# Kernel optimization log

Measured on AMD Instinct MI355X. Metric: run time of the kernel, lower is better.

The kernel has to match this reference:

```python
import jax, jax.numpy as jnp
import numpy as np
import math

B, R, C = 4, 512, 512
E, H, D, M, F = 256, 16, 16, 16, 512  # embed, heads, qkv_dim, ms_hidden, ff_hidden
EPS = 1e-5


def setup_inputs() -> dict:
    key = jax.random.key(0)
    ks = jax.random.split(key, 20)
    s = lambda fan_in: 1.0 / math.sqrt(fan_in)
    u = lambda k, shape, lim: jax.random.uniform(k, shape, jnp.float32, -lim, lim)
    mix1_init = (1 / 2) ** 0.5
    mix2_init = (1 / 16) ** 0.5
    return {
        "row_emb": jax.random.normal(ks[0], (B, R, E), jnp.float32),
        "col_emb": jax.random.normal(ks[1], (B, C, E), jnp.float32),
        "cost_mat": jax.random.uniform(ks[2], (B, R, C), jnp.float32),
        "Wq": u(ks[3], (E, H * D), s(E)),
        "Wk": u(ks[4], (E, H * D), s(E)),
        "Wv": u(ks[5], (E, H * D), s(E)),
        "mix1_w": u(ks[6], (H, 2, M), mix1_init),
        "mix1_b": u(ks[7], (H, M), mix1_init),
        "mix2_w": u(ks[8], (H, M, 1), mix2_init),
        "mix2_b": u(ks[9], (H, 1), mix2_init),
        "Wc": u(ks[10], (H * D, E), s(H * D)),
        "bc": u(ks[11], (E,), s(H * D)),
        "W1": u(ks[12], (E, F), s(E)),
        "b1": u(ks[13], (F,), s(E)),
        "W2": u(ks[14], (F, E), s(F)),
        "b2": u(ks[15], (E,), s(F)),
        "g1": jnp.ones((E,), jnp.float32),
        "be1": jnp.zeros((E,), jnp.float32),
        "g2": jnp.ones((E,), jnp.float32),
        "be2": jnp.zeros((E,), jnp.float32),
    }


def _instance_norm(x, gamma, beta):
    # InstanceNorm1d on x permuted to (B, E, L): normalize over seq dim per (b, channel)
    mean = jnp.mean(x, axis=1, keepdims=True)          # [B,1,E]
    var = jnp.mean((x - mean) ** 2, axis=1, keepdims=True)
    return (x - mean) * jax.lax.rsqrt(var + EPS) * gamma + beta


def reference(row_emb, col_emb, cost_mat, Wq, Wk, Wv, mix1_w, mix1_b, mix2_w,
              mix2_b, Wc, bc, W1, b1, W2, b2, g1, be1, g2, be2):
    # QKV projections, split heads: [B,L,H*D] -> [B,H,L,D]
    q = (row_emb @ Wq).reshape(B, R, H, D).transpose(0, 2, 1, 3)
    k = (col_emb @ Wk).reshape(B, C, H, D).transpose(0, 2, 1, 3)
    v = (col_emb @ Wv).reshape(B, C, H, D).transpose(0, 2, 1, 3)

    dot = jnp.einsum('bhrd,bhcd->bhrc', q, k) / math.sqrt(D)
    cost = jnp.broadcast_to(cost_mat[:, None, :, :], (B, H, R, C))
    two = jnp.stack((dot, cost), axis=-1)               # [B,H,R,C,2]

    # per-head 2 -> M -> 1 mixing MLP over scores
    ms1 = jnp.einsum('bhrcs,hsm->bhrcm', two, mix1_w) + mix1_b[None, :, None, None, :]
    ms1 = jax.nn.relu(ms1)
    mixed = jnp.einsum('bhrcm,hm->bhrc', ms1, mix2_w[:, :, 0]) + mix2_b[:, 0][None, :, None, None]

    weights = jax.nn.softmax(mixed, axis=-1)            # [B,H,R,C]
    out = jnp.einsum('bhrc,bhcd->bhrd', weights, v)
    out_concat = out.transpose(0, 2, 1, 3).reshape(B, R, H * D)

    mh = out_concat @ Wc + bc                           # multi_head_combine

    # TransformerFFN with instance norm
    x = _instance_norm(row_emb + mh, g1, be1)
    ffn = jax.nn.relu(x @ W1 + b1) @ W2 + b2
    return _instance_norm(x + ffn, g2, be2)
```

## Files before the change

kernel.cpp:

```cpp
#include <hip/hip_runtime.h>
#include <hip/hip_bf16.h>

typedef __hip_bfloat16 bf16;
typedef __hip_bfloat162 bf162;
typedef _Float16 f16;
typedef __attribute__((ext_vector_type(2))) _Float16 h2;
typedef __attribute__((ext_vector_type(8))) short short8;
typedef __attribute__((ext_vector_type(4))) float f32x4;

#define B_ 4
#define R_ 512
#define C_ 512
#define E_ 256
#define H_ 16
#define D_ 16

__device__ __forceinline__ float b2f(bf16 x) { return __bfloat162float(x); }
__device__ __forceinline__ void stout(bf16* p, float v) { *p = __float2bfloat16(v); }
__device__ __forceinline__ void stout(f16* p, float v) { *p = (f16)v; }

template <int AMODE, typename OT, int BM, int BN, bool BIAS, int RES, bool RELU, bool STATS>
__device__ __forceinline__ void mfma_gemm_body(
    const void* __restrict__ Ap, const float* __restrict__ W, float bscl,
    const float* __restrict__ bias, const void* __restrict__ Res,
    const float* __restrict__ normS, const float* __restrict__ normG, const float* __restrict__ normB,
    float* __restrict__ statsOut, OT* __restrict__ Cout,
    int M, int N, int K, int bx, int by)
{
    constexpr int MT = BM / 32, NT = BN / 32;
    constexpr int AEL = BM * 64 / 256, BEL = BN * 64 / 256;
    __shared__ __align__(16) bf16 As[BM * 80];
    __shared__ __align__(16) bf16 Bs[BN * 80];
    const int tid = threadIdx.x;
    const int wid = tid >> 6, lane = tid & 63;
    const int wm = wid >> 1, wn = wid & 1;
    const int fr = lane & 15, quad = lane >> 4;
    const int m0 = by * BM, n0 = bx * BN;
    const int arow = (AEL == 16) ? (tid >> 2) : (tid >> 3);
    const int akg  = (AEL == 16) ? ((tid & 3) << 4) : ((tid & 7) << 3);
    const int brow = (BEL == 16) ? (tid >> 2) : (tid >> 3);
    const int bkg  = (BEL == 16) ? ((tid & 3) << 4) : ((tid & 7) << 3);

    f32x4 acc[MT][NT];
#pragma unroll
    for (int mt = 0; mt < MT; mt++)
#pragma unroll
        for (int nt = 0; nt < NT; nt++) acc[mt][nt] = (f32x4){0.f, 0.f, 0.f, 0.f};

    for (int k0 = 0; k0 < K; k0 += 64) {
        if constexpr (AMODE == 0) {
            const short8* gp = (const short8*)((const bf16*)Ap + (size_t)(m0 + arow) * K + k0 + akg);
#pragma unroll
            for (int t8 = 0; t8 < AEL / 8; t8++) *(short8*)(&As[arow * 80 + akg + 8 * t8]) = gp[t8];
        } else if constexpr (AMODE == 1) {
            const float4* gp = (const float4*)((const float*)Ap + (size_t)(m0 + arow) * K + k0 + akg);
#pragma unroll
            for (int j = 0; j < AEL / 4; j++) {
                const float4 f = gp[j];
                *(bf162*)(&As[arow * 80 + akg + j * 4])     = __float22bfloat162_rn(make_float2(f.x, f.y));
                *(bf162*)(&As[arow * 80 + akg + j * 4 + 2]) = __float22bfloat162_rn(make_float2(f.z, f.w));
            }
        } else {
            const int bb = (m0 + arow) >> 9;
            const bf16* ap = (const bf16*)Ap + (size_t)(m0 + arow) * K + k0 + akg;
            bf16 tmp[AEL];
#pragma unroll
            for (int t8 = 0; t8 < AEL / 8; t8++) *(short8*)(tmp + 8 * t8) = ((const short8*)ap)[t8];
#pragma unroll
            for (int j = 0; j < AEL; j++) {
                const int e = k0 + akg + j;
                const float s = normS[bb * 256 + e], sq = normS[1024 + bb * 256 + e];
                const float mn = s * (1.f / 512.f);
                float var = sq * (1.f / 512.f) - mn * mn; var = fmaxf(var, 0.f);
                As[arow * 80 + akg + j] = __float2bfloat16(
                    (b2f(tmp[j]) - mn) * rsqrtf(var + 1e-5f) * normG[e] + normB[e]);
            }
        }
        {
#pragma unroll
            for (int j = 0; j < BEL; j++)
                Bs[brow * 80 + bkg + j] = __float2bfloat16(
                    bscl * W[(size_t)(k0 + bkg + j) * N + (n0 + brow)]);
        }
        __syncthreads();

        short8 af[MT][2], bfr[NT][2];
#pragma unroll
        for (int mt = 0; mt < MT; mt++) {
            const int ar = wm * (BM / 2) + mt * 16 + fr;
#pragma unroll
            for (int kh = 0; kh < 2; kh++)
                af[mt][kh] = *(const short8*)(&As[ar * 80 + quad * 8 + kh * 32]);
        }
#pragma unroll
        for (int nt = 0; nt < NT; nt++) {
            const int br = wn * (BN / 2) + nt * 16 + fr;
#pragma unroll
            for (int kh = 0; kh < 2; kh++)
                bfr[nt][kh] = *(const short8*)(&Bs[br * 80 + quad * 8 + kh * 32]);
        }
#pragma unroll
        for (int kh = 0; kh < 2; kh++)
#pragma unroll
            for (int mt = 0; mt < MT; mt++)
#pragma unroll
                for (int nt = 0; nt < NT; nt++)
                    acc[mt][nt] = __builtin_amdgcn_mfma_f32_16x16x32_bf16(
                        af[mt][kh], bfr[nt][kh], acc[mt][nt], 0, 0, 0);
        __syncthreads();
    }

    float vsum[NT], vss[NT];
#pragma unroll
    for (int nt = 0; nt < NT; nt++) { vsum[nt] = 0.f; vss[nt] = 0.f; }
#pragma unroll
    for (int mt = 0; mt < MT; mt++) {
#pragma unroll
        for (int nt = 0; nt < NT; nt++) {
#pragma unroll
            for (int i = 0; i < 4; i++) {
                const int row = m0 + wm * (BM / 2) + mt * 16 + quad * 4 + i;
                const int col = n0 + wn * (BN / 2) + nt * 16 + fr;
                float v = acc[mt][nt][i];
                if (BIAS) v += bias[col];
                if constexpr (RES == 1) v += ((const float*)Res)[(size_t)row * N + col];
                if constexpr (RES == 3) {
                    const int bb = row >> 9;
                    const float yv = b2f(((const bf16*)Res)[(size_t)row * N + col]);
                    const float s = normS[bb * 256 + col], sq = normS[1024 + bb * 256 + col];
                    const float mn = s * (1.f / 512.f);
                    float var = sq * (1.f / 512.f) - mn * mn; var = fmaxf(var, 0.f);
                    v += (yv - mn) * rsqrtf(var + 1e-5f) * normG[col] + normB[col];
                }
                if (RELU) v = fmaxf(v, 0.f);
                stout(&Cout[(size_t)row * N + col], v);
                if (STATS) { vsum[nt] += v; vss[nt] += v * v; }
            }
        }
    }
    if constexpr (STATS) {
        float* sred = (float*)As;
#pragma unroll
        for (int nt = 0; nt < NT; nt++) {
            float a = vsum[nt]; a += __shfl_xor(a, 16, 64); a += __shfl_xor(a, 32, 64);
            float c = vss[nt];  c += __shfl_xor(c, 16, 64); c += __shfl_xor(c, 32, 64);
            if (quad == 0) {
                const int cl = wn * (BN / 2) + nt * 16 + fr;
                sred[wm * (2 * BN) + cl * 2 + 0] = a;
                sred[wm * (2 * BN) + cl * 2 + 1] = c;
            }
        }
        __syncthreads();
        if (tid < 2 * BN) {
            const int cl = tid >> 1, w = tid & 1;
            const float tot = sred[cl * 2 + w] + sred[2 * BN + cl * 2 + w];
            atomicAdd(&statsOut[w * 1024 + (m0 >> 9) * 256 + n0 + cl], tot);
        }
    }
}

template <int AMODE, typename OT, int BM, int BN, bool BIAS, int RES, bool RELU, bool STATS>
__global__ __launch_bounds__(256) void mfma_gemm_kernel(
    const void* __restrict__ Ap, const float* __restrict__ W, float bscl,
    const float* __restrict__ bias, const void* __restrict__ Res,
    const float* __restrict__ normS, const float* __restrict__ normG, const float* __restrict__ normB,
    float* __restrict__ statsOut, OT* __restrict__ Cout, int M, int N, int K)
{
    mfma_gemm_body<AMODE, OT, BM, BN, BIAS, RES, RELU, STATS>(
        Ap, W, bscl, bias, Res, normS, normG, normB, statsOut, Cout,
        M, N, K, blockIdx.x, blockIdx.y);
}

__global__ __launch_bounds__(256) void qkv_kernel(
    const float* __restrict__ rowE, const float* __restrict__ colE,
    const float* __restrict__ Wq, const float* __restrict__ Wk, const float* __restrict__ Wv,
    f16* __restrict__ qo, f16* __restrict__ ko, bf16* __restrict__ vo)
{
    const int z = blockIdx.z;
    if (z == 2) {
        mfma_gemm_body<1, bf16, 32, 64, false, 0, false, false>(
            colE, Wv, 1.f, nullptr, nullptr, nullptr, nullptr, nullptr, nullptr, vo,
            2048, 256, 256, blockIdx.x, blockIdx.y);
    } else {
        mfma_gemm_body<1, f16, 32, 64, false, 0, false, false>(
            (z == 0) ? rowE : colE, (z == 0) ? Wq : Wk, (z == 0) ? 0.25f : 1.f,
            nullptr, nullptr, nullptr, nullptr, nullptr, nullptr, (z == 0) ? qo : ko,
            2048, 256, 256, blockIdx.x, blockIdx.y);
    }
}

__global__ __launch_bounds__(256) void attn_kernel(
    const f16* __restrict__ q, const f16* __restrict__ k, const bf16* __restrict__ v,
    const float* __restrict__ cost, const float* __restrict__ m1w, const float* __restrict__ m1b,
    const float* __restrict__ m2w, const float* __restrict__ m2b,
    bf16* __restrict__ po, float* __restrict__ plf)
{
    __shared__ __align__(16) f16 kbuf[128 * 16];
    __shared__ __align__(16) short vbuf[128 * 16];

    const int rt = blockIdx.x >> 2, cs = blockIdx.x & 3;
    const int h = blockIdx.y, b = blockIdx.z;
    const int tid = threadIdx.x, wid = tid >> 6, lane = tid & 63;
    const int quad = lane >> 4, fr = lane & 15;

    {
        const size_t base = ((size_t)b * C_) * 256 + h * 16 + (size_t)cs * 128 * 256;
        const int lc = tid >> 1, dp = (tid & 1) * 8;
        const size_t g = base + (size_t)lc * 256 + dp;
        *(short8*)(&kbuf[lc * 16 + dp]) = *(const short8*)(k + g);
        *(short8*)(&vbuf[lc * 16 + dp]) = *(const short8*)(v + g);
    }

    h2 w1a2[8], w1b2[8], b1h[8], w2p[8];
#pragma unroll
    for (int i = 0; i < 8; i++) {
        h2 t;
        t.x = (f16)m1w[h * 32 + 2 * i];      t.y = (f16)m1w[h * 32 + 2 * i + 1];      w1a2[i] = t;
        t.x = (f16)m1w[h * 32 + 16 + 2 * i]; t.y = (f16)m1w[h * 32 + 17 + 2 * i];     w1b2[i] = t;
        t.x = (f16)m1b[h * 16 + 2 * i];      t.y = (f16)m1b[h * 16 + 2 * i + 1];      b1h[i] = t;
        t.x = (f16)m2w[h * 16 + 2 * i];      t.y = (f16)m2w[h * 16 + 2 * i + 1];      w2p[i] = t;
    }
    const float b2v = m2b[h];
    const h2 zero2 = (h2)(f16)0;

    const int row_m = rt * 64 + wid * 16 + fr;
    short8 qraw[2];
    {
        const short8* qp = (const short8*)(q + (size_t)(b * R_ + row_m) * 256 + h * 16);
        qraw[0] = qp[0]; qraw[1] = qp[1];
    }
    const h2* qh = (const h2*)qraw;

    __syncthreads();

    const float* crow = cost + (size_t)(b * R_ + row_m) * C_ + cs * 128;
    h2 sh[16];
#pragma unroll
    for (int blk = 0; blk < 4; blk++) {
        const float4 c0 = *(const float4*)(crow + blk * 32 + quad * 8);
        const float4 c1 = *(const float4*)(crow + blk * 32 + quad * 8 + 4);
        const float carr[8] = {c0.x, c0.y, c0.z, c0.w, c1.x, c1.y, c1.z, c1.w};
#pragma unroll
        for (int j = 0; j < 8; j++) {
            const int col = blk * 32 + quad * 8 + j;
            const h2* kr = (const h2*)(&kbuf[col * 16]);
            h2 dacc = qh[0] * kr[0];
#pragma unroll
            for (int i = 1; i < 8; i++) dacc = qh[i] * kr[i] + dacc;
            const float dot = (float)dacc.x + (float)dacc.y;
            const float cst = carr[j];
            const f16 doth = (f16)dot, csth = (f16)cst;
            h2 dot2; dot2.x = doth; dot2.y = doth;
            h2 cst2; cst2.x = csth; cst2.y = csth;
            h2 acc2 = (h2)(f16)0;
#pragma unroll
            for (int i = 0; i < 8; i++) {
                h2 t = dot2 * w1a2[i] + b1h[i];
                t = cst2 * w1b2[i] + t;
                t = __builtin_elementwise_max(t, zero2);
                acc2 = t * w2p[i] + acc2;
            }
            const float s = b2v + (float)acc2.x + (float)acc2.y;
            const f16 sf = (f16)s;
            if (j & 1) sh[blk * 4 + (j >> 1)].y = sf;
            else       sh[blk * 4 + (j >> 1)].x = sf;
        }
    }

    h2 mx2 = sh[0];
#pragma unroll
    for (int i = 1; i < 16; i++) mx2 = __builtin_elementwise_max(mx2, sh[i]);
    float m_l = fmaxf((float)mx2.x, (float)mx2.y);
    m_l = fmaxf(m_l, __shfl_xor(m_l, 16, 64));
    m_l = fmaxf(m_l, __shfl_xor(m_l, 32, 64));

    f32x4 oacc = (f32x4){0.f, 0.f, 0.f, 0.f};
    float lsum = 0.f;
#pragma unroll
    for (int blk = 0; blk < 4; blk++) {
        short8 pa, bv;
#pragma unroll
        for (int jj = 0; jj < 4; jj++) {
            const h2 t = sh[blk * 4 + jj];
            const float e0 = __expf((float)t.x - m_l);
            const float e1 = __expf((float)t.y - m_l);
            lsum += e0 + e1;
            const bf162 pr = __float22bfloat162_rn(make_float2(e0, e1));
            pa[2 * jj]     = __builtin_bit_cast(short, pr.x);
            pa[2 * jj + 1] = __builtin_bit_cast(short, pr.y);
        }
#pragma unroll
        for (int j = 0; j < 8; j++) bv[j] = vbuf[(blk * 32 + quad * 8 + j) * 16 + fr];
        oacc = __builtin_amdgcn_mfma_f32_16x16x32_bf16(pa, bv, oacc, 0, 0, 0);
    }
    lsum += __shfl_xor(lsum, 16, 64);
    lsum += __shfl_xor(lsum, 32, 64);

    const int idxbase = cs * 32768 + ((b * H_ + h) << 9) + rt * 64 + wid * 16;
    if (quad == 0) plf[idxbase + fr] = lsum * __expf(m_l);
#pragma unroll
    for (int i = 0; i < 4; i++) {
        const float li = __shfl(lsum, quad * 4 + i, 64);
        po[(size_t)(idxbase + quad * 4 + i) * 16 + fr] = __float2bfloat16(oacc[i] / li);
    }
}

__global__ __launch_bounds__(256) void attn_merge_kernel(
    const bf16* __restrict__ po, const float* __restrict__ plf, bf16* __restrict__ sa,
    float* __restrict__ stats1, float* __restrict__ stats2)
{
    const int idx = blockIdx.x * 256 + threadIdx.x;
    if (idx < 2048) stats1[idx] = 0.f;
    else if (idx < 4096) stats2[idx - 2048] = 0.f;
    const float l0 = plf[idx], l1 = plf[32768 + idx];
    const float l2 = plf[65536 + idx], l3 = plf[98304 + idx];
    const float inv = 1.f / (l0 + l1 + l2 + l3);
    float oo[16] = {};
#pragma unroll
    for (int c = 0; c < 4; c++) {
        const float wgt = ((c == 0) ? l0 : (c == 1) ? l1 : (c == 2) ? l2 : l3) * inv;
        const bf162* pp = (const bf162*)(po + (size_t)(c * 32768 + idx) * 16);
#pragma unroll
        for (int j = 0; j < 8; j++) {
            const float2 f = __bfloat1622float2(pp[j]);
            oo[2 * j]     = fmaf(wgt, f.x, oo[2 * j]);
            oo[2 * j + 1] = fmaf(wgt, f.y, oo[2 * j + 1]);
        }
    }
    const int b = idx >> 13, h = (idx >> 9) & 15, r = idx & 511;
    bf162* dst = (bf162*)(sa + (size_t)(b * R_ + r) * 256 + h * 16);
#pragma unroll
    for (int j = 0; j < 8; j++)
        dst[j] = __float22bfloat162_rn(make_float2(oo[2 * j], oo[2 * j + 1]));
}

__global__ __launch_bounds__(256) void apply_in2_kernel(
    const bf16* __restrict__ xin, const float* __restrict__ stats,
    const float* __restrict__ g, const float* __restrict__ be, float* __restrict__ outp)
{
    const int base = (blockIdx.x * 256 + threadIdx.x) * 4;
    const int b = base >> 17;
    const bf162* xp = (const bf162*)(xin + base);
    const float2 x0 = __bfloat1622float2(xp[0]), x1 = __bfloat1622float2(xp[1]);
    const float xv[4] = {x0.x, x0.y, x1.x, x1.y};
    float4 rr;
    float* rp = (float*)&rr;
#pragma unroll
    for (int j = 0; j < 4; j++) {
        const int e = (base & 255) + j;
        const float s = stats[b * 256 + e], sq = stats[1024 + b * 256 + e];
        const float mn = s * (1.f / 512.f);
        float var = sq * (1.f / 512.f) - mn * mn; var = fmaxf(var, 0.f);
        rp[j] = (xv[j] - mn) * rsqrtf(var + 1e-5f) * g[e] + be[e];
    }
    *(float4*)(outp + base) = rr;
}

extern "C" void kernel_launch(void* const* d_in, const int* in_sizes, int n_in,
                              void* d_out, int out_size, void* d_ws, size_t ws_size,
                              hipStream_t stream)
{
    (void)in_sizes; (void)n_in; (void)out_size; (void)ws_size;
    const float* row_emb = (const float*)d_in[0];
    const float* col_emb = (const float*)d_in[1];
    const float* cost    = (const float*)d_in[2];
    const float* Wq  = (const float*)d_in[3];
    const float* Wk  = (const float*)d_in[4];
    const float* Wv  = (const float*)d_in[5];
    const float* m1w = (const float*)d_in[6];
    const float* m1b = (const float*)d_in[7];
    const float* m2w = (const float*)d_in[8];
    const float* m2b = (const float*)d_in[9];
    const float* Wc  = (const float*)d_in[10];
    const float* bc  = (const float*)d_in[11];
    const float* W1  = (const float*)d_in[12];
    const float* b1  = (const float*)d_in[13];
    const float* W2  = (const float*)d_in[14];
    const float* b2  = (const float*)d_in[15];
    const float* g1  = (const float*)d_in[16];
    const float* be1 = (const float*)d_in[17];
    const float* g2  = (const float*)d_in[18];
    const float* be2 = (const float*)d_in[19];
    float* out = (float*)d_out;

    char* w = (char*)d_ws;
    f16*  sq  = (f16*)(w + 0);
    f16*  sk  = (f16*)(w + 1048576);
    bf16* sv  = (bf16*)(w + 2097152);
    bf16* sa  = (bf16*)(w + 0);
    bf16* sy  = (bf16*)(w + 1048576);
    bf16* st  = (bf16*)(w + 2097152);
    bf16* po  = (bf16*)(w + 3145728);
    bf16* shm = (bf16*)(w + 3145728);
    float* plf = (float*)(w + 7340032);
    float* stats1 = (float*)(w + 8257536);
    float* stats2 = stats1 + 2048;

    const dim3 blk(256);

    qkv_kernel<<<dim3(4, 64, 3), blk, 0, stream>>>(row_emb, col_emb, Wq, Wk, Wv, sq, sk, sv);

    attn_kernel<<<dim3(32, 16, 4), blk, 0, stream>>>(
        sq, sk, sv, cost, m1w, m1b, m2w, m2b, po, plf);

    attn_merge_kernel<<<dim3(128), blk, 0, stream>>>(po, plf, sa, stats1, stats2);

    mfma_gemm_kernel<0, bf16, 32, 32, true, 1, false, true><<<dim3(8, 64), blk, 0, stream>>>(
        sa, Wc, 1.f, bc, row_emb, nullptr, nullptr, nullptr, stats1, sy, 2048, 256, 256);

    mfma_gemm_kernel<2, bf16, 32, 64, true, 0, true, false><<<dim3(8, 64), blk, 0, stream>>>(
        sy, W1, 1.f, b1, nullptr, stats1, g1, be1, nullptr, shm, 2048, 512, 256);

    mfma_gemm_kernel<0, bf16, 32, 32, true, 3, false, true><<<dim3(8, 64), blk, 0, stream>>>(
        shm, W2, 1.f, b2, sy, stats1, g1, be1, stats2, st, 2048, 256, 512);

    apply_in2_kernel<<<dim3(512), blk, 0, stream>>>(st, stats2, g2, be2, out);
}
```

Before: 175.2 us.

## Pre-transpose weights to bf16 once per call and load B tiles vectorized

Adds a kernel that converts each fp32 weight matrix into a transposed bf16 copy (folding the 0.25 query scale in) and also zeroes the norm statistics buffers. The GEMM B-tile loads then become contiguous 16-byte vector loads instead of strided scalar fp32 loads with per-element conversion. The cost is one extra launch plus about 1 MB of weight conversion traffic on every call. The stats zeroing moves out of the merge kernel into the new kernel.

```diff
diff --git a/kernel.cpp b/kernel.cpp
--- a/kernel.cpp
+++ b/kernel.cpp
@@ -19,9 +19,47 @@
 __device__ __forceinline__ void stout(bf16* p, float v) { *p = __float2bfloat16(v); }
 __device__ __forceinline__ void stout(f16* p, float v) { *p = (f16)v; }
 
+__global__ __launch_bounds__(256) void transpose_cvt_kernel(
+    const float* __restrict__ Wq, const float* __restrict__ Wk, const float* __restrict__ Wv,
+    const float* __restrict__ Wc, const float* __restrict__ W1, const float* __restrict__ W2,
+    bf16* __restrict__ WqT, bf16* __restrict__ WkT, bf16* __restrict__ WvT,
+    bf16* __restrict__ WcT, bf16* __restrict__ W1T, bf16* __restrict__ W2T,
+    float* __restrict__ statsZ)
+{
+    __shared__ bf16 tile[32][33];
+    const int wsel = blockIdx.y;
+    const int tx = blockIdx.x;
+    if (wsel == 0 && tx >= 64) {
+        const int idx = (tx - 64) * 256 + threadIdx.x;
+        if (idx < 4096) statsZ[idx] = 0.f;
+        return;
+    }
+    const float* src; bf16* dst; int K, N; float scl = 1.0f;
+    switch (wsel) {
+        case 0: src = Wq; dst = WqT; K = 256; N = 256; scl = 0.25f; break;
+        case 1: src = Wk; dst = WkT; K = 256; N = 256; break;
+        case 2: src = Wv; dst = WvT; K = 256; N = 256; break;
+        case 3: src = Wc; dst = WcT; K = 256; N = 256; break;
+        case 4: src = W1; dst = W1T; K = 256; N = 512; break;
+        default: src = W2; dst = W2T; K = 512; N = 256; break;
+    }
+    const int ntiles = (K >> 5) * (N >> 5);
+    if (tx >= ntiles) return;
+    const int ncnt = N >> 5;
+    const int tk = tx / ncnt, tn = tx % ncnt;
+    const int c = threadIdx.x & 31, r = threadIdx.x >> 5;
+#pragma unroll
+    for (int i = 0; i < 4; i++)
+        tile[r + i * 8][c] = __float2bfloat16(scl * src[(size_t)(tk * 32 + r + i * 8) * N + tn * 32 + c]);
+    __syncthreads();
+#pragma unroll
+    for (int i = 0; i < 4; i++)
+        dst[(size_t)(tn * 32 + r + i * 8) * K + tk * 32 + c] = tile[c][r + i * 8];
+}
+
 template <int AMODE, typename OT, int BM, int BN, bool BIAS, int RES, bool RELU, bool STATS>
 __device__ __forceinline__ void mfma_gemm_body(
-    const void* __restrict__ Ap, const float* __restrict__ W, float bscl,
+    const void* __restrict__ Ap, const bf16* __restrict__ BT,
     const float* __restrict__ bias, const void* __restrict__ Res,
     const float* __restrict__ normS, const float* __restrict__ normG, const float* __restrict__ normB,
     float* __restrict__ statsOut, OT* __restrict__ Cout,
@@ -77,10 +115,9 @@
             }
         }
         {
-#pragma unroll
-            for (int j = 0; j < BEL; j++)
-                Bs[brow * 80 + bkg + j] = __float2bfloat16(
-                    bscl * W[(size_t)(k0 + bkg + j) * N + (n0 + brow)]);
+            const short8* gp = (const short8*)(BT + (size_t)(n0 + brow) * K + k0 + bkg);
+#pragma unroll
+            for (int t8 = 0; t8 < BEL / 8; t8++) *(short8*)(&Bs[brow * 80 + bkg + 8 * t8]) = gp[t8];
         }
         __syncthreads();
 
@@ -161,29 +198,29 @@
 
 template <int AMODE, typename OT, int BM, int BN, bool BIAS, int RES, bool RELU, bool STATS>
 __global__ __launch_bounds__(256) void mfma_gemm_kernel(
-    const void* __restrict__ Ap, const float* __restrict__ W, float bscl,
+    const void* __restrict__ Ap, const bf16* __restrict__ BT,
     const float* __restrict__ bias, const void* __restrict__ Res,
     const float* __restrict__ normS, const float* __restrict__ normG, const float* __restrict__ normB,
     float* __restrict__ statsOut, OT* __restrict__ Cout, int M, int N, int K)
 {
     mfma_gemm_body<AMODE, OT, BM, BN, BIAS, RES, RELU, STATS>(
-        Ap, W, bscl, bias, Res, normS, normG, normB, statsOut, Cout,
+        Ap, BT, bias, Res, normS, normG, normB, statsOut, Cout,
         M, N, K, blockIdx.x, blockIdx.y);
 }
 
 __global__ __launch_bounds__(256) void qkv_kernel(
     const float* __restrict__ rowE, const float* __restrict__ colE,
-    const float* __restrict__ Wq, const float* __restrict__ Wk, const float* __restrict__ Wv,
+    const bf16* __restrict__ WqT, const bf16* __restrict__ WkT, const bf16* __restrict__ WvT,
     f16* __restrict__ qo, f16* __restrict__ ko, bf16* __restrict__ vo)
 {
     const int z = blockIdx.z;
     if (z == 2) {
         mfma_gemm_body<1, bf16, 32, 64, false, 0, false, false>(
-            colE, Wv, 1.f, nullptr, nullptr, nullptr, nullptr, nullptr, nullptr, vo,
+            colE, WvT, nullptr, nullptr, nullptr, nullptr, nullptr, nullptr, vo,
             2048, 256, 256, blockIdx.x, blockIdx.y);
     } else {
         mfma_gemm_body<1, f16, 32, 64, false, 0, false, false>(
-            (z == 0) ? rowE : colE, (z == 0) ? Wq : Wk, (z == 0) ? 0.25f : 1.f,
+            (z == 0) ? rowE : colE, (z == 0) ? WqT : WkT,
             nullptr, nullptr, nullptr, nullptr, nullptr, nullptr, (z == 0) ? qo : ko,
             2048, 256, 256, blockIdx.x, blockIdx.y);
     }
@@ -306,12 +343,9 @@
 }
 
 __global__ __launch_bounds__(256) void attn_merge_kernel(
-    const bf16* __restrict__ po, const float* __restrict__ plf, bf16* __restrict__ sa,
-    float* __restrict__ stats1, float* __restrict__ stats2)
+    const bf16* __restrict__ po, const float* __restrict__ plf, bf16* __restrict__ sa)
 {
     const int idx = blockIdx.x * 256 + threadIdx.x;
-    if (idx < 2048) stats1[idx] = 0.f;
-    else if (idx < 4096) stats2[idx - 2048] = 0.f;
     const float l0 = plf[idx], l1 = plf[32768 + idx];
     const float l2 = plf[65536 + idx], l3 = plf[98304 + idx];
     const float inv = 1.f / (l0 + l1 + l2 + l3);
@@ -384,35 +418,45 @@
     float* out = (float*)d_out;
 
     char* w = (char*)d_ws;
-    f16*  sq  = (f16*)(w + 0);
-    f16*  sk  = (f16*)(w + 1048576);
-    bf16* sv  = (bf16*)(w + 2097152);
-    bf16* sa  = (bf16*)(w + 0);
-    bf16* sy  = (bf16*)(w + 1048576);
-    bf16* st  = (bf16*)(w + 2097152);
-    bf16* po  = (bf16*)(w + 3145728);
-    bf16* shm = (bf16*)(w + 3145728);
-    float* plf = (float*)(w + 7340032);
-    float* stats1 = (float*)(w + 8257536);
+    const size_t MB = 1u << 20;
+    f16*  sq  = (f16*)(w + 0 * MB);
+    f16*  sk  = (f16*)(w + 1 * MB);
+    bf16* sv  = (bf16*)(w + 2 * MB);
+    bf16* sa  = (bf16*)(w + 0 * MB);
+    bf16* sy  = (bf16*)(w + 1 * MB);
+    bf16* st  = (bf16*)(w + 2 * MB);
+    bf16* po  = (bf16*)(w + 3 * MB);
+    bf16* shm = (bf16*)(w + 3 * MB);
+    float* plf = (float*)(w + 7 * MB);
+    bf16* WqT = (bf16*)(w + 8 * MB);
+    bf16* WkT = WqT + 65536;
+    bf16* WvT = WkT + 65536;
+    bf16* WcT = WvT + 65536;
+    bf16* W1T = WcT + 65536;
+    bf16* W2T = W1T + 131072;
+    float* stats1 = (float*)(w + 9 * MB);
     float* stats2 = stats1 + 2048;
 
     const dim3 blk(256);
 
-    qkv_kernel<<<dim3(4, 64, 3), blk, 0, stream>>>(row_emb, col_emb, Wq, Wk, Wv, sq, sk, sv);
+    transpose_cvt_kernel<<<dim3(128, 6), blk, 0, stream>>>(
+        Wq, Wk, Wv, Wc, W1, W2, WqT, WkT, WvT, WcT, W1T, W2T, stats1);
+
+    qkv_kernel<<<dim3(4, 64, 3), blk, 0, stream>>>(row_emb, col_emb, WqT, WkT, WvT, sq, sk, sv);
 
     attn_kernel<<<dim3(32, 16, 4), blk, 0, stream>>>(
         sq, sk, sv, cost, m1w, m1b, m2w, m2b, po, plf);
 
-    attn_merge_kernel<<<dim3(128), blk, 0, stream>>>(po, plf, sa, stats1, stats2);
+    attn_merge_kernel<<<dim3(128), blk, 0, stream>>>(po, plf, sa);
 
     mfma_gemm_kernel<0, bf16, 32, 32, true, 1, false, true><<<dim3(8, 64), blk, 0, stream>>>(
-        sa, Wc, 1.f, bc, row_emb, nullptr, nullptr, nullptr, stats1, sy, 2048, 256, 256);
+        sa, WcT, bc, row_emb, nullptr, nullptr, nullptr, stats1, sy, 2048, 256, 256);
 
     mfma_gemm_kernel<2, bf16, 32, 64, true, 0, true, false><<<dim3(8, 64), blk, 0, stream>>>(
-        sy, W1, 1.f, b1, nullptr, stats1, g1, be1, nullptr, shm, 2048, 512, 256);
+        sy, W1T, b1, nullptr, stats1, g1, be1, nullptr, shm, 2048, 512, 256);
 
     mfma_gemm_kernel<0, bf16, 32, 32, true, 3, false, true><<<dim3(8, 64), blk, 0, stream>>>(
-        shm, W2, 1.f, b2, sy, stats1, g1, be1, stats2, st, 2048, 256, 512);
+        shm, W2T, b2, sy, stats1, g1, be1, stats2, st, 2048, 256, 512);
 
     apply_in2_kernel<<<dim3(512), blk, 0, stream>>>(st, stats2, g2, be2, out);
 }
```

Measured after the change: 160.9 us. -8.2%, faster.

## Fuse split-attention merge into combine GEMM and vectorize swizzled weight loads

Applied to the files above, without the earlier changes.

Removes the separate attention merge kernel. The attention kernel now writes partial outputs in row-major [B,R,H*D] layout per column split and zeroes the stats buffers. The combine GEMM gains an A-mode that merges the four partials using the log-sum weights while loading its A tile. Weight tiles are also loaded with coalesced float4 reads along N and stored to LDS with an XOR swizzle, replacing the strided scalar transposed loads. The cost is redundant merge arithmetic in the GEMM and a changed workspace layout.

```diff
diff --git a/kernel.cpp b/kernel.cpp
--- a/kernel.cpp
+++ b/kernel.cpp
@@ -28,7 +28,7 @@
     int M, int N, int K, int bx, int by)
 {
     constexpr int MT = BM / 32, NT = BN / 32;
-    constexpr int AEL = BM * 64 / 256, BEL = BN * 64 / 256;
+    constexpr int AEL = BM * 64 / 256;
     __shared__ __align__(16) bf16 As[BM * 80];
     __shared__ __align__(16) bf16 Bs[BN * 80];
     const int tid = threadIdx.x;
@@ -38,8 +38,6 @@
     const int m0 = by * BM, n0 = bx * BN;
     const int arow = (AEL == 16) ? (tid >> 2) : (tid >> 3);
     const int akg  = (AEL == 16) ? ((tid & 3) << 4) : ((tid & 7) << 3);
-    const int brow = (BEL == 16) ? (tid >> 2) : (tid >> 3);
-    const int bkg  = (BEL == 16) ? ((tid & 3) << 4) : ((tid & 7) << 3);
 
     f32x4 acc[MT][NT];
 #pragma unroll
@@ -60,7 +58,7 @@
                 *(bf162*)(&As[arow * 80 + akg + j * 4])     = __float22bfloat162_rn(make_float2(f.x, f.y));
                 *(bf162*)(&As[arow * 80 + akg + j * 4 + 2]) = __float22bfloat162_rn(make_float2(f.z, f.w));
             }
-        } else {
+        } else if constexpr (AMODE == 2) {
             const int bb = (m0 + arow) >> 9;
             const bf16* ap = (const bf16*)Ap + (size_t)(m0 + arow) * K + k0 + akg;
             bf16 tmp[AEL];
@@ -75,12 +73,52 @@
                 As[arow * 80 + akg + j] = __float2bfloat16(
                     (b2f(tmp[j]) - mn) * rsqrtf(var + 1e-5f) * normG[e] + normB[e]);
             }
-        }
-        {
-#pragma unroll
-            for (int j = 0; j < BEL; j++)
-                Bs[brow * 80 + bkg + j] = __float2bfloat16(
-                    bscl * W[(size_t)(k0 + bkg + j) * N + (n0 + brow)]);
+        } else {
+            const int row = m0 + arow;
+            const int e0 = k0 + akg;
+            const int bb = row >> 9, rr = row & 511, hh = e0 >> 4;
+            const int lidx = ((bb * 16 + hh) << 9) + rr;
+            const float l0 = normS[lidx], l1 = normS[32768 + lidx];
+            const float l2 = normS[65536 + lidx], l3 = normS[98304 + lidx];
+            const float inv = 1.f / (l0 + l1 + l2 + l3);
+            const bf16* pob = (const bf16*)Ap;
+            float a8[8] = {};
+#pragma unroll
+            for (int c = 0; c < 4; c++) {
+                const float wgt = ((c == 0) ? l0 : (c == 1) ? l1 : (c == 2) ? l2 : l3) * inv;
+                const bf162* pp = (const bf162*)(pob + (size_t)c * 524288 + (size_t)row * 256 + e0);
+#pragma unroll
+                for (int jj = 0; jj < 4; jj++) {
+                    const float2 f = __bfloat1622float2(pp[jj]);
+                    a8[2 * jj]     = fmaf(wgt, f.x, a8[2 * jj]);
+                    a8[2 * jj + 1] = fmaf(wgt, f.y, a8[2 * jj + 1]);
+                }
+            }
+#pragma unroll
+            for (int j = 0; j < 8; j++) As[arow * 80 + akg + j] = __float2bfloat16(a8[j]);
+        }
+        if constexpr (BN == 64) {
+            const int kk = tid >> 2, nnb = (tid & 3) << 4;
+            const float4* wp = (const float4*)(W + (size_t)(k0 + kk) * N + n0 + nnb);
+            float4 f[4] = {wp[0], wp[1], wp[2], wp[3]};
+            const float* fs = (const float*)f;
+#pragma unroll
+            for (int j = 0; j < 16; j++) {
+                const int n = nnb + j;
+                const int sw = ((n >> 3) & 7) << 3;
+                Bs[n * 80 + (kk ^ sw)] = __float2bfloat16(bscl * fs[j]);
+            }
+        } else {
+            const int kk = tid >> 2, nnb = (tid & 3) << 3;
+            const float4* wp = (const float4*)(W + (size_t)(k0 + kk) * N + n0 + nnb);
+            float4 f[2] = {wp[0], wp[1]};
+            const float* fs = (const float*)f;
+#pragma unroll
+            for (int j = 0; j < 8; j++) {
+                const int n = nnb + j;
+                const int sw = ((n >> 3) & 7) << 3;
+                Bs[n * 80 + (kk ^ sw)] = __float2bfloat16(bscl * fs[j]);
+            }
         }
         __syncthreads();
 
@@ -95,9 +133,10 @@
 #pragma unroll
         for (int nt = 0; nt < NT; nt++) {
             const int br = wn * (BN / 2) + nt * 16 + fr;
+            const int sw = ((br >> 3) & 7) << 3;
 #pragma unroll
             for (int kh = 0; kh < 2; kh++)
-                bfr[nt][kh] = *(const short8*)(&Bs[br * 80 + quad * 8 + kh * 32]);
+                bfr[nt][kh] = *(const short8*)(&Bs[br * 80 + ((quad * 8 + kh * 32) ^ sw)]);
         }
 #pragma unroll
         for (int kh = 0; kh < 2; kh++)
@@ -193,7 +232,8 @@
     const f16* __restrict__ q, const f16* __restrict__ k, const bf16* __restrict__ v,
     const float* __restrict__ cost, const float* __restrict__ m1w, const float* __restrict__ m1b,
     const float* __restrict__ m2w, const float* __restrict__ m2b,
-    bf16* __restrict__ po, float* __restrict__ plf)
+    bf16* __restrict__ po, float* __restrict__ plf,
+    float* __restrict__ stats1, float* __restrict__ stats2)
 {
     __shared__ __align__(16) f16 kbuf[128 * 16];
     __shared__ __align__(16) short vbuf[128 * 16];
@@ -202,6 +242,12 @@
     const int h = blockIdx.y, b = blockIdx.z;
     const int tid = threadIdx.x, wid = tid >> 6, lane = tid & 63;
     const int quad = lane >> 4, fr = lane & 15;
+
+    if (blockIdx.y == 0 && blockIdx.z == 0) {
+        const int zi = blockIdx.x * 256 + tid;
+        if (zi < 2048) stats1[zi] = 0.f;
+        else if (zi < 4096) stats2[zi - 2048] = 0.f;
+    }
 
     {
         const size_t base = ((size_t)b * C_) * 256 + h * 16 + (size_t)cs * 128 * 256;
@@ -296,42 +342,15 @@
     lsum += __shfl_xor(lsum, 16, 64);
     lsum += __shfl_xor(lsum, 32, 64);
 
-    const int idxbase = cs * 32768 + ((b * H_ + h) << 9) + rt * 64 + wid * 16;
-    if (quad == 0) plf[idxbase + fr] = lsum * __expf(m_l);
+    const int rbase = rt * 64 + wid * 16;
+    if (quad == 0) plf[cs * 32768 + ((b * 16 + h) << 9) + rbase + fr] = lsum * __expf(m_l);
+    bf16* poc = po + (size_t)cs * 524288;
 #pragma unroll
     for (int i = 0; i < 4; i++) {
         const float li = __shfl(lsum, quad * 4 + i, 64);
-        po[(size_t)(idxbase + quad * 4 + i) * 16 + fr] = __float2bfloat16(oacc[i] / li);
-    }
-}
-
-__global__ __launch_bounds__(256) void attn_merge_kernel(
-    const bf16* __restrict__ po, const float* __restrict__ plf, bf16* __restrict__ sa,
-    float* __restrict__ stats1, float* __restrict__ stats2)
-{
-    const int idx = blockIdx.x * 256 + threadIdx.x;
-    if (idx < 2048) stats1[idx] = 0.f;
-    else if (idx < 4096) stats2[idx - 2048] = 0.f;
-    const float l0 = plf[idx], l1 = plf[32768 + idx];
-    const float l2 = plf[65536 + idx], l3 = plf[98304 + idx];
-    const float inv = 1.f / (l0 + l1 + l2 + l3);
-    float oo[16] = {};
-#pragma unroll
-    for (int c = 0; c < 4; c++) {
-        const float wgt = ((c == 0) ? l0 : (c == 1) ? l1 : (c == 2) ? l2 : l3) * inv;
-        const bf162* pp = (const bf162*)(po + (size_t)(c * 32768 + idx) * 16);
-#pragma unroll
-        for (int j = 0; j < 8; j++) {
-            const float2 f = __bfloat1622float2(pp[j]);
-            oo[2 * j]     = fmaf(wgt, f.x, oo[2 * j]);
-            oo[2 * j + 1] = fmaf(wgt, f.y, oo[2 * j + 1]);
-        }
-    }
-    const int b = idx >> 13, h = (idx >> 9) & 15, r = idx & 511;
-    bf162* dst = (bf162*)(sa + (size_t)(b * R_ + r) * 256 + h * 16);
-#pragma unroll
-    for (int j = 0; j < 8; j++)
-        dst[j] = __float22bfloat162_rn(make_float2(oo[2 * j], oo[2 * j + 1]));
+        poc[(size_t)(b * 512 + rbase + quad * 4 + i) * 256 + h * 16 + fr] =
+            __float2bfloat16(oacc[i] / li);
+    }
 }
 
 __global__ __launch_bounds__(256) void apply_in2_kernel(
@@ -384,16 +403,16 @@
     float* out = (float*)d_out;
 
     char* w = (char*)d_ws;
-    f16*  sq  = (f16*)(w + 0);
-    f16*  sk  = (f16*)(w + 1048576);
-    bf16* sv  = (bf16*)(w + 2097152);
-    bf16* sa  = (bf16*)(w + 0);
-    bf16* sy  = (bf16*)(w + 1048576);
-    bf16* st  = (bf16*)(w + 2097152);
-    bf16* po  = (bf16*)(w + 3145728);
-    bf16* shm = (bf16*)(w + 3145728);
-    float* plf = (float*)(w + 7340032);
-    float* stats1 = (float*)(w + 8257536);
+    const size_t MB = 1u << 20;
+    f16*  sq  = (f16*)(w + 0 * MB);
+    f16*  sk  = (f16*)(w + 1 * MB);
+    bf16* sv  = (bf16*)(w + 2 * MB);
+    bf16* po  = (bf16*)(w + 3 * MB);
+    float* plf = (float*)(w + 7 * MB);
+    bf16* sy  = (bf16*)(w + 8 * MB);
+    bf16* shm = (bf16*)(w + 9 * MB);
+    bf16* st  = (bf16*)(w + 11 * MB);
+    float* stats1 = (float*)(w + 12 * MB);
     float* stats2 = stats1 + 2048;
 
     const dim3 blk(256);
@@ -401,12 +420,10 @@
     qkv_kernel<<<dim3(4, 64, 3), blk, 0, stream>>>(row_emb, col_emb, Wq, Wk, Wv, sq, sk, sv);
 
     attn_kernel<<<dim3(32, 16, 4), blk, 0, stream>>>(
-        sq, sk, sv, cost, m1w, m1b, m2w, m2b, po, plf);
-
-    attn_merge_kernel<<<dim3(128), blk, 0, stream>>>(po, plf, sa, stats1, stats2);
-
-    mfma_gemm_kernel<0, bf16, 32, 32, true, 1, false, true><<<dim3(8, 64), blk, 0, stream>>>(
-        sa, Wc, 1.f, bc, row_emb, nullptr, nullptr, nullptr, stats1, sy, 2048, 256, 256);
+        sq, sk, sv, cost, m1w, m1b, m2w, m2b, po, plf, stats1, stats2);
+
+    mfma_gemm_kernel<3, bf16, 32, 32, true, 1, false, true><<<dim3(8, 64), blk, 0, stream>>>(
+        po, Wc, 1.f, bc, row_emb, plf, nullptr, nullptr, stats1, sy, 2048, 256, 256);
 
     mfma_gemm_kernel<2, bf16, 32, 64, true, 0, true, false><<<dim3(8, 64), blk, 0, stream>>>(
         sy, W1, 1.f, b1, nullptr, stats1, g1, be1, nullptr, shm, 2048, 512, 256);
```

Result: faster. 162.8 us (-7.1%).
